# Optimization experiments

Hardware: AMD Instinct MI355X
Metric: run time of the kernel (lower is better)

Reference implementation:

```python
import jax, jax.numpy as jnp
import numpy as np

EMB_DIM = 128
DEC_DIM = 128
NEG_INF = -1e10


def setup_inputs() -> dict:
    key = jax.random.key(0)
    k1, k2, k3, k4, k5, k6 = jax.random.split(key, 6)
    B, S = 64, 4096
    hidden = jax.random.normal(k1, (B, DEC_DIM), dtype=jnp.float32)
    seq_embs = jax.random.normal(k2, (S, B, EMB_DIM), dtype=jnp.float32)
    mask = jax.random.randint(k3, (B, S), 0, 2, dtype=jnp.int32)
    # nn.Linear(emb_dim + dec_dim, dec_dim): weight [dec_dim, emb_dim+dec_dim]
    fan_in = EMB_DIM + DEC_DIM
    bound = 1.0 / np.sqrt(fan_in)
    W_attn = jax.random.uniform(k4, (DEC_DIM, fan_in), minval=-bound, maxval=bound, dtype=jnp.float32)
    b_attn = jax.random.uniform(k5, (DEC_DIM,), minval=-bound, maxval=bound, dtype=jnp.float32)
    # nn.Linear(dec_dim, 1, bias=False): weight [1, dec_dim]
    bound_v = 1.0 / np.sqrt(DEC_DIM)
    v_w = jax.random.uniform(k6, (1, DEC_DIM), minval=-bound_v, maxval=bound_v, dtype=jnp.float32)
    return {"hidden": hidden, "seq_embs": seq_embs, "mask": mask,
            "W_attn": W_attn, "b_attn": b_attn, "v_w": v_w}


def reference(hidden, seq_embs, mask, W_attn, b_attn, v_w):
    # hidden: [B, Dd]; seq_embs: [S, B, De]; mask: [B, S]
    # Concat order in torch is (hidden, seq_embs) -> split W accordingly.
    Wh = W_attn[:, :DEC_DIM]   # [Dd, Dd] applied to hidden
    We = W_attn[:, DEC_DIM:]   # [Dd, De] applied to seq_embs
    embs = jnp.transpose(seq_embs, (1, 0, 2))            # [B, S, De]
    # energy = tanh(Linear(cat(hidden, embs))) without materializing concat
    h_proj = hidden @ Wh.T + b_attn                       # [B, Dd]
    e_proj = jnp.einsum('bse,de->bsd', embs, We)          # [B, S, Dd]
    energy = jnp.tanh(h_proj[:, None, :] + e_proj)        # [B, S, Dd]
    attention = jnp.einsum('bsd,d->bs', energy, v_w[0])   # [B, S]
    attention = jnp.where(mask == 0, NEG_INF, attention)
    return jax.nn.softmax(attention, axis=1)
```

## Files before the change

kernel.cpp:

```cpp
#include <hip/hip_runtime.h>
#include <hip/hip_bf16.h>

#define BB 64
#define SS 4096
#define EE 128
#define DD 128
#define FAN 256
#define TILES 2
#define ROWS (TILES * 64)
#define GG (SS / ROWS)

typedef __bf16 bf16x8 __attribute__((ext_vector_type(8)));
typedef unsigned short u16x8 __attribute__((ext_vector_type(8)));
typedef float f32x4 __attribute__((ext_vector_type(4)));

__device__ inline bf16x8 ld_frag_lds(const unsigned char* p) {
    union { u16x8 u; bf16x8 b; } c;
    c.u = *(const u16x8*)p;
    return c.b;
}

__device__ inline uint2 f4_to_bf4(float4 f) {
    union { __hip_bfloat162 b; unsigned u; } lo, hi;
    lo.b = __float22bfloat162_rn(make_float2(f.x, f.y));
    hi.b = __float22bfloat162_rn(make_float2(f.z, f.w));
    return make_uint2(lo.u, hi.u);
}

__device__ inline float tanh_fast(float x) {
    float ax = fabsf(x);
    float e = __expf(-2.0f * ax);
    float t = (1.0f - e) * __builtin_amdgcn_rcpf(1.0f + e);
    return x < 0.0f ? -t : t;
}

__global__ __launch_bounds__(256) void prep_kernel(
        const float* __restrict__ hidden, const float* __restrict__ W_attn,
        const float* __restrict__ b_attn, const float* __restrict__ v_w,
        float* __restrict__ hproj, unsigned char* __restrict__ Wb,
        float* __restrict__ v_out) {
    const int b = blockIdx.x;
    const int t = threadIdx.x;
    if (t < 128) {
        float acc = b_attn[t];
        const float4* hrow = (const float4*)(hidden + b * DD);
        const float4* wrow = (const float4*)(W_attn + t * FAN);
        #pragma unroll
        for (int e = 0; e < 32; e++) {
            float4 h = hrow[e], w = wrow[e];
            acc += h.x * w.x + h.y * w.y + h.z * w.z + h.w * w.w;
        }
        hproj[b * DD + t] = acc;
        if (b == 0) v_out[t] = v_w[t];
    } else {
        int tt = t - 128;
        int d  = 2 * b + (tt >> 6);
        int e0 = (tt & 63) * 2;
        float2 src = *(const float2*)(W_attn + d * FAN + DD + e0);
        union { __hip_bfloat162 bb; unsigned u; } c;
        c.bb = __float22bfloat162_rn(src);
        unsigned off = (unsigned)(d * 256)
                     + (((unsigned)(e0 * 2)) ^ (((unsigned)d & 7u) << 4));
        *(unsigned*)(Wb + off) = c.u;
    }
}

__global__ __launch_bounds__(256, 4) void logits_kernel(
        const float* __restrict__ seq_embs, const int* __restrict__ mask,
        const float* __restrict__ hproj, const unsigned char* __restrict__ Wb,
        const float* __restrict__ v, float* __restrict__ out,
        float* __restrict__ psums) {
    __shared__ __attribute__((aligned(1024))) unsigned char Ws[DD * EE * 2];

    const int b    = blockIdx.y;
    const int g    = blockIdx.x;
    const int tid  = threadIdx.x;
    const int wave = tid >> 6;
    const int lane = tid & 63;
    const int m    = lane & 15;
    const int quad = lane >> 4;
    const int arow = wave * 16 + m;

    #pragma unroll
    for (int j = 0; j < 8; j++) {
        const int c = wave * 8 + j;
        __builtin_amdgcn_global_load_lds(
            (const __attribute__((address_space(1))) unsigned int*)(Wb + c * 1024 + lane * 16),
            (__attribute__((address_space(3))) unsigned int*)(Ws + c * 1024),
            16, 0, 0);
    }

    const int* __restrict__ mask_g = mask + (size_t)b * SS + g * ROWS;
    const float* __restrict__ xbase = seq_embs
        + (size_t)(g * ROWS + arow) * (BB * EE)
        + (size_t)b * EE + quad * 8;

    int am[2];
    int4 mq[2];
    bf16x8 af[2][4];
    {
        am[0] = mask_g[arow];
        mq[0] = *(const int4*)(mask_g + wave * 16 + quad * 4);
        const float* xrow = xbase;
        #pragma unroll
        for (int kk = 0; kk < 4; kk++) {
            union { uint4 q; bf16x8 bf; } c;
            c.q = make_uint4(0u, 0u, 0u, 0u);
            if (am[0] != 0) {
                float4 f0 = *(const float4*)(xrow + kk * 32);
                float4 f1 = *(const float4*)(xrow + kk * 32 + 4);
                uint2 a = f4_to_bf4(f0), bq = f4_to_bf4(f1);
                c.q = make_uint4(a.x, a.y, bq.x, bq.y);
            }
            af[0][kk] = c.bf;
        }
    }

    float hp_r[8], v_r[8];
    #pragma unroll
    for (int t = 0; t < 8; t++) {
        hp_r[t] = hproj[b * DD + t * 16 + m];
        v_r[t]  = v[t * 16 + m];
    }

    __syncthreads();

    const unsigned sw = ((unsigned)(m & 7)) << 4;
    float blocksum = 0.0f;

    #pragma unroll
    for (int tile = 0; tile < TILES; tile++) {
        const int cur = tile & 1;
        if (tile + 1 < TILES) {
            const int nxt = cur ^ 1;
            am[nxt] = mask_g[(tile + 1) * 64 + arow];
            mq[nxt] = *(const int4*)(mask_g + (tile + 1) * 64 + wave * 16 + quad * 4);
            const float* xrow = xbase + (size_t)((tile + 1) * 64) * (BB * EE);
            #pragma unroll
            for (int kk = 0; kk < 4; kk++) {
                union { uint4 q; bf16x8 bf; } c;
                c.q = make_uint4(0u, 0u, 0u, 0u);
                if (am[nxt] != 0) {
                    float4 f0 = *(const float4*)(xrow + kk * 32);
                    float4 f1 = *(const float4*)(xrow + kk * 32 + 4);
                    uint2 a = f4_to_bf4(f0), bq = f4_to_bf4(f1);
                    c.q = make_uint4(a.x, a.y, bq.x, bq.y);
                }
                af[nxt][kk] = c.bf;
            }
        }

        f32x4 acc[8];
        #pragma unroll
        for (int t = 0; t < 8; t++) acc[t] = (f32x4){0.f, 0.f, 0.f, 0.f};
        #pragma unroll
        for (int kk = 0; kk < 4; kk++) {
            const unsigned cb = ((unsigned)(kk * 64 + quad * 16)) ^ sw;
            #pragma unroll
            for (int t = 0; t < 8; t++) {
                bf16x8 bf = ld_frag_lds(Ws + (unsigned)((t * 16 + m) * 256) + cb);
                acc[t] = __builtin_amdgcn_mfma_f32_16x16x32_bf16(af[cur][kk], bf, acc[t], 0, 0, 0);
            }
        }

        const int mqa[4] = {mq[cur].x, mq[cur].y, mq[cur].z, mq[cur].w};
        float red[4];
        #pragma unroll
        for (int r = 0; r < 4; r++) {
            float red_r = 0.0f;
            if (mqa[r] != 0) {
                float part = 0.f;
                #pragma unroll
                for (int t = 0; t < 8; t++)
                    part += v_r[t] * tanh_fast(hp_r[t] + acc[t][r]);
                part += __shfl_xor(part, 1);
                part += __shfl_xor(part, 2);
                part += __shfl_xor(part, 4);
                part += __shfl_xor(part, 8);
                red_r = __expf(part);
            }
            red[r] = red_r;
            blocksum += red_r;
        }
        if (m == 0) {
            *(float4*)&out[(size_t)b * SS + g * ROWS + tile * 64
                           + wave * 16 + quad * 4] =
                make_float4(red[0], red[1], red[2], red[3]);
        }
    }

    blocksum += __shfl_xor(blocksum, 16);
    blocksum += __shfl_xor(blocksum, 32);
    if (lane == 0) psums[(b * GG + g) * 4 + wave] = blocksum;
}

__global__ __launch_bounds__(256) void norm_kernel(
        float* __restrict__ out, const float* __restrict__ psums) {
    const int b = blockIdx.y;
    const int tid = threadIdx.x;
    const int lane = tid & 63;
    float p = psums[b * 128 + lane] + psums[b * 128 + 64 + lane];
    #pragma unroll
    for (int off = 32; off >= 1; off >>= 1)
        p += __shfl_xor(p, off);
    const float inv = 1.0f / p;
    const int i = (blockIdx.x * 256 + tid) * 4;
    float4 v = *(float4*)&out[(size_t)b * SS + i];
    v.x *= inv; v.y *= inv; v.z *= inv; v.w *= inv;
    *(float4*)&out[(size_t)b * SS + i] = v;
}

extern "C" void kernel_launch(void* const* d_in, const int* in_sizes, int n_in,
                              void* d_out, int out_size, void* d_ws, size_t ws_size,
                              hipStream_t stream) {
    const float* hidden   = (const float*)d_in[0];
    const float* seq_embs = (const float*)d_in[1];
    const int*   mask     = (const int*)d_in[2];
    const float* W_attn   = (const float*)d_in[3];
    const float* b_attn   = (const float*)d_in[4];
    const float* v_w      = (const float*)d_in[5];
    float* out = (float*)d_out;

    float*         hproj = (float*)d_ws;
    unsigned char* Wb    = (unsigned char*)d_ws + 32768;
    float*         vv    = (float*)((char*)d_ws + 65536);
    float*         psums = (float*)((char*)d_ws + 66048);

    prep_kernel<<<64, 256, 0, stream>>>(hidden, W_attn, b_attn, v_w, hproj, Wb, vv);
    dim3 grid(GG, BB);
    logits_kernel<<<grid, 256, 0, stream>>>(seq_embs, mask, hproj, Wb, vv, out, psums);
    dim3 ngrid(SS / (256 * 4), BB);
    norm_kernel<<<ngrid, 256, 0, stream>>>(out, psums);
}
```

Measured before the change: 221.9 us.

## Fuse softmax normalization into logits kernel via last-block atomic counter

Removes the separate norm kernel. Each logits block bumps a per-batch atomic counter, and the last block to finish for that batch sums the partial sums and rescales the whole output row. Tiles per block also double, which halves the grid and the number of partial sums per batch. This saves one kernel launch and a full pass over the output. In exchange the final normalization runs serially in one block per batch, and the larger tiles reduce parallelism.

```diff
diff --git a/kernel.cpp b/kernel.cpp
--- a/kernel.cpp
+++ b/kernel.cpp
@@ -6,7 +6,7 @@
 #define EE 128
 #define DD 128
 #define FAN 256
-#define TILES 2
+#define TILES 4
 #define ROWS (TILES * 64)
 #define GG (SS / ROWS)
 
@@ -38,9 +38,10 @@
         const float* __restrict__ hidden, const float* __restrict__ W_attn,
         const float* __restrict__ b_attn, const float* __restrict__ v_w,
         float* __restrict__ hproj, unsigned char* __restrict__ Wb,
-        float* __restrict__ v_out) {
+        float* __restrict__ v_out, unsigned* __restrict__ cnt) {
     const int b = blockIdx.x;
     const int t = threadIdx.x;
+    if (t == 0) cnt[b * 32] = 0u;
     if (t < 128) {
         float acc = b_attn[t];
         const float4* hrow = (const float4*)(hidden + b * DD);
@@ -69,7 +70,7 @@
         const float* __restrict__ seq_embs, const int* __restrict__ mask,
         const float* __restrict__ hproj, const unsigned char* __restrict__ Wb,
         const float* __restrict__ v, float* __restrict__ out,
-        float* __restrict__ psums) {
+        float* __restrict__ psums, unsigned* __restrict__ cnt) {
     __shared__ __attribute__((aligned(1024))) unsigned char Ws[DD * EE * 2];
 
     const int b    = blockIdx.y;
@@ -192,22 +193,35 @@
     blocksum += __shfl_xor(blocksum, 16);
     blocksum += __shfl_xor(blocksum, 32);
     if (lane == 0) psums[(b * GG + g) * 4 + wave] = blocksum;
-}
-
-__global__ __launch_bounds__(256) void norm_kernel(
-        float* __restrict__ out, const float* __restrict__ psums) {
-    const int b = blockIdx.y;
-    const int tid = threadIdx.x;
-    const int lane = tid & 63;
-    float p = psums[b * 128 + lane] + psums[b * 128 + 64 + lane];
-    #pragma unroll
-    for (int off = 32; off >= 1; off >>= 1)
-        p += __shfl_xor(p, off);
-    const float inv = 1.0f / p;
-    const int i = (blockIdx.x * 256 + tid) * 4;
-    float4 v = *(float4*)&out[(size_t)b * SS + i];
-    v.x *= inv; v.y *= inv; v.z *= inv; v.w *= inv;
-    *(float4*)&out[(size_t)b * SS + i] = v;
+
+    __threadfence();
+    __syncthreads();
+    volatile int*   s_last = (volatile int*)&Ws[0];
+    volatile float* s_inv  = (volatile float*)&Ws[4];
+    if (tid == 0) {
+        unsigned old = atomicAdd(&cnt[b * 32], 1u);
+        *s_last = (old == (unsigned)(GG - 1)) ? 1 : 0;
+    }
+    __syncthreads();
+    if (*s_last) {
+        __threadfence();
+        if (tid < 64) {
+            float p = psums[b * 64 + tid];
+            #pragma unroll
+            for (int off = 32; off >= 1; off >>= 1)
+                p += __shfl_xor(p, off);
+            if (tid == 0) *s_inv = 1.0f / p;
+        }
+        __syncthreads();
+        const float inv = *s_inv;
+        float* row = out + (size_t)b * SS;
+        #pragma unroll
+        for (int i = 0; i < 4; i++) {
+            float4 vv4 = *(float4*)&row[(size_t)(i * 256 + tid) * 4];
+            vv4.x *= inv; vv4.y *= inv; vv4.z *= inv; vv4.w *= inv;
+            *(float4*)&row[(size_t)(i * 256 + tid) * 4] = vv4;
+        }
+    }
 }
 
 extern "C" void kernel_launch(void* const* d_in, const int* in_sizes, int n_in,
@@ -225,10 +239,9 @@
     unsigned char* Wb    = (unsigned char*)d_ws + 32768;
     float*         vv    = (float*)((char*)d_ws + 65536);
     float*         psums = (float*)((char*)d_ws + 66048);
-
-    prep_kernel<<<64, 256, 0, stream>>>(hidden, W_attn, b_attn, v_w, hproj, Wb, vv);
+    unsigned*      cnt   = (unsigned*)((char*)d_ws + 82432);
+
+    prep_kernel<<<64, 256, 0, stream>>>(hidden, W_attn, b_attn, v_w, hproj, Wb, vv, cnt);
     dim3 grid(GG, BB);
-    logits_kernel<<<grid, 256, 0, stream>>>(seq_embs, mask, hproj, Wb, vv, out, psums);
-    dim3 ngrid(SS / (256 * 4), BB);
-    norm_kernel<<<ngrid, 256, 0, stream>>>(out, psums);
-}
+    logits_kernel<<<grid, 256, 0, stream>>>(seq_embs, mask, hproj, Wb, vv, out, psums, cnt);
+}
```

Result: slower. 315.5 us (+42.2%).
